# Performance work log

Measured on AMD Instinct MI355X. Metric: run time of the kernel, lower is better.

Reference implementation:

```python
import jax, jax.numpy as jnp
import numpy as np

V, D, H, L, FF, NC = 32000, 512, 8, 4, 2048, 10
HD = D // H
EPS = 1e-5


def _layernorm(x, g, b):
    m = jnp.mean(x, axis=-1, keepdims=True)
    v = jnp.mean((x - m) ** 2, axis=-1, keepdims=True)
    return (x - m) * jax.lax.rsqrt(v + EPS) * g + b


def _pos_encoding(T, d):
    pos = jnp.arange(T, dtype=jnp.float32)[:, None]
    div = jnp.exp(jnp.arange(0, d, 2, dtype=jnp.float32) * (-np.log(10000.0) / d))
    pe = jnp.zeros((T, d), dtype=jnp.float32)
    pe = pe.at[:, 0::2].set(jnp.sin(pos * div))
    pe = pe.at[:, 1::2].set(jnp.cos(pos * div))
    return pe


def setup_inputs() -> dict:
    key = jax.random.key(0)
    ks = iter(jax.random.split(key, 32))
    n = lambda shape, s=0.02: jax.random.normal(next(ks), shape, dtype=jnp.float32) * s
    inp = {
        "tokens": jax.random.randint(next(ks), (8, 1024), 0, V),
        "emb": n((V, D), 1.0),
        # attention projections, stored (in, out) so y = x @ W + b
        "Wq": n((L, D, D)), "bq": jnp.zeros((L, D)),
        "Wk": n((L, D, D)), "bk": jnp.zeros((L, D)),
        "Wv": n((L, D, D)), "bv": jnp.zeros((L, D)),
        "Wo": n((L, D, D)), "bo": jnp.zeros((L, D)),
        "ln1_g": jnp.ones((L, D)), "ln1_b": jnp.zeros((L, D)),
        "ln2_g": jnp.ones((L, D)), "ln2_b": jnp.zeros((L, D)),
        "W1": n((L, D, FF)), "b1": jnp.zeros((L, FF)),
        "W2": n((L, FF, D)), "b2": jnp.zeros((L, D)),
        "heavy_w": n((D, D)), "heavy_b": jnp.zeros((D,)),
        "heavy_a1": n((D, D)), "heavy_a2": n((D, D)),
        "norm_g": jnp.ones((D,)), "norm_b": jnp.zeros((D,)),
        "cls_W": n((D, NC)), "cls_b": jnp.zeros((NC,)),
    }
    return inp


def reference(tokens, emb, Wq, bq, Wk, bk, Wv, bv, Wo, bo,
              ln1_g, ln1_b, ln2_g, ln2_b, W1, b1, W2, b2,
              heavy_w, heavy_b, heavy_a1, heavy_a2,
              norm_g, norm_b, cls_W, cls_b):
    B, T = tokens.shape
    x = emb[tokens] + _pos_encoding(T, D)[None]  # [B,T,D]
    scale = 1.0 / np.sqrt(HD)
    for l in range(L):
        # attention block (pre-norm)
        h = _layernorm(x, ln1_g[l], ln1_b[l])
        q = (h @ Wq[l] + bq[l]).reshape(B, T, H, HD)
        k = (h @ Wk[l] + bk[l]).reshape(B, T, H, HD)
        v = (h @ Wv[l] + bv[l]).reshape(B, T, H, HD)
        scores = jnp.einsum("bqhd,bkhd->bhqk", q, k) * scale
        attn = jax.nn.softmax(scores, axis=-1)
        o = jnp.einsum("bhqk,bkhd->bqhd", attn, v).reshape(B, T, D)
        x = x + (o @ Wo[l] + bo[l])
        # feedforward block
        h = _layernorm(x, ln2_g[l], ln2_b[l])
        x = x + (jax.nn.gelu(h @ W1[l] + b1[l], approximate=False) @ W2[l] + b2[l])
    # heavy layer: chained matmuls + bias + tanh (vectorized over B*T)
    x = jnp.tanh(((x @ heavy_w) @ heavy_a1) @ heavy_a2 + heavy_b)
    x = _layernorm(x, norm_g, norm_b)
    x = jnp.mean(x, axis=1)  # [B,D]
    return x @ cls_W + cls_b  # [B,NC]
```

## Files before the change

kernel.cpp:

```cpp
#include <hip/hip_runtime.h>
#include <math.h>

#define BS   8
#define TT   1024
#define DD   512
#define HH   8
#define LL   4
#define FFD  2048
#define NCC  10
#define MM   (BS*TT)
#define MDl  ((long)MM*DD)

typedef unsigned short u16;
typedef short  short8 __attribute__((ext_vector_type(8)));
typedef float  f32x4  __attribute__((ext_vector_type(4)));
typedef u16    u16x8  __attribute__((ext_vector_type(8)));
typedef u16    u16x4  __attribute__((ext_vector_type(4)));

static __device__ __forceinline__ u16 f2b(float f) {
    union { float f; unsigned u; } x; x.f = f;
    unsigned r = x.u + 0x7FFFu + ((x.u >> 16) & 1u);
    return (u16)(r >> 16);
}
static __device__ __forceinline__ u16 f2b_fast(float f) {
    union { float f; unsigned u; } x; x.f = f;
    return (u16)((x.u + 0x8000u) >> 16);
}
static __device__ __forceinline__ float b2f(u16 u) {
    union { unsigned u; float f; } x; x.u = ((unsigned)u) << 16;
    return x.f;
}

__global__ __launch_bounds__(256)
void embed_kernel(const int* __restrict__ tok, const float* __restrict__ emb,
                  float* __restrict__ X) {
    int i = blockIdx.x * 256 + threadIdx.x;
    int d = i & (DD - 1);
    int row = i >> 9;
    int t = row & (TT - 1);
    int j = d >> 1;
    float freq = __expf((float)(2 * j) * (-9.210340371976184f / 512.0f));
    float ang = (float)t * freq;
    float pe = (d & 1) ? cosf(ang) : sinf(ang);
    X[i] = emb[(long)tok[row] * DD + d] + pe;
}

template<int OUTBF>
__global__ __launch_bounds__(256)
void ln_kernel(const float* __restrict__ in, void* __restrict__ outp,
               const float* __restrict__ g, const float* __restrict__ b) {
    int row = blockIdx.x;
    int tid = threadIdx.x;
    const float* x = in + (long)row * DD;
    float x1 = x[tid], x2 = x[tid + 256];
    __shared__ float red[256], red2[256];
    red[tid] = x1 + x2;
    red2[tid] = x1 * x1 + x2 * x2;
    __syncthreads();
    for (int st = 128; st > 0; st >>= 1) {
        if (tid < st) { red[tid] += red[tid + st]; red2[tid] += red2[tid + st]; }
        __syncthreads();
    }
    float mean = red[0] * (1.0f / DD);
    float var = red2[0] * (1.0f / DD) - mean * mean;
    float rstd = rsqrtf(var + 1e-5f);
    float y1 = (x1 - mean) * rstd * g[tid] + b[tid];
    float y2 = (x2 - mean) * rstd * g[tid + 256] + b[tid + 256];
    if (OUTBF) {
        u16* o = (u16*)outp + (long)row * DD;
        o[tid] = f2b(y1); o[tid + 256] = f2b(y2);
    } else {
        float* o = (float*)outp + (long)row * DD;
        o[tid] = y1; o[tid + 256] = y2;
    }
}

template<int OUTBF, int HAS_BIAS, int ACT, int HAS_RES>
__global__ __launch_bounds__(512, 2)
void mfma_gemm(const u16* __restrict__ A, const u16* __restrict__ BT,
               const float* __restrict__ bias, const float* __restrict__ R,
               void* __restrict__ Cout, int N, int K) {
    __shared__ __align__(16) u16 lds[17408];
    u16* As = lds;
    u16* Bs = lds + 8192;
    const int tid = threadIdx.x;
    const int lane = tid & 63;
    const int w = tid >> 6;
    const int wm = w >> 1;
    const int wn = w & 1;
    const long bm = (long)blockIdx.y * 128;
    const long bn = (long)blockIdx.x * 128;

    f32x4 acc[2][4];
#pragma unroll
    for (int i = 0; i < 2; ++i)
#pragma unroll
        for (int j = 0; j < 4; ++j) acc[i][j] = {0.f, 0.f, 0.f, 0.f};

    const int srow = tid >> 2;
    const int sc0 = (tid & 3) * 2;
    const u16* Ag = A + (bm + srow) * K + sc0 * 8;
    const u16* Bg = BT + (bn + srow) * K + sc0 * 8;
    int soff[2];
#pragma unroll
    for (int j = 0; j < 2; ++j)
        soff[j] = srow * 64 + ((sc0 + j) ^ (srow & 7)) * 8;

    const int fr = lane & 15;
    const int g = lane >> 4;
    const int am0 = wm * 32 + fr;
    const int bn0 = wn * 64 + fr;
    const int sw = fr & 7;

    u16x8 sa[2][2], sb[2][2];
#pragma unroll
    for (int j = 0; j < 2; ++j) {
        sa[0][j] = *(const u16x8*)(Ag + j * 8);
        sb[0][j] = *(const u16x8*)(Bg + j * 8);
    }

    for (int k0 = 0; k0 < K; k0 += 128) {
#pragma unroll
        for (int half = 0; half < 2; ++half) {
            const int cb = half, nb = half ^ 1;
            __syncthreads();
#pragma unroll
            for (int j = 0; j < 2; ++j) {
                *(u16x8*)&As[soff[j]] = sa[cb][j];
                *(u16x8*)&Bs[soff[j]] = sb[cb][j];
            }
            const int knext = k0 + (half + 1) * 64;
            if (knext < K) {
#pragma unroll
                for (int j = 0; j < 2; ++j) {
                    sa[nb][j] = *(const u16x8*)(Ag + knext + j * 8);
                    sb[nb][j] = *(const u16x8*)(Bg + knext + j * 8);
                }
            }
            __syncthreads();
#pragma unroll
            for (int kk = 0; kk < 2; ++kk) {
                const int pos = ((kk << 2) + g) ^ sw;
                short8 af[2], bfv[4];
#pragma unroll
                for (int mi = 0; mi < 2; ++mi)
                    af[mi] = *(const short8*)&As[(am0 + mi * 16) * 64 + pos * 8];
#pragma unroll
                for (int ni = 0; ni < 4; ++ni)
                    bfv[ni] = *(const short8*)&Bs[(bn0 + ni * 16) * 64 + pos * 8];
#pragma unroll
                for (int mi = 0; mi < 2; ++mi)
#pragma unroll
                    for (int ni = 0; ni < 4; ++ni)
                        acc[mi][ni] = __builtin_amdgcn_mfma_f32_16x16x32_bf16(
                            af[mi], bfv[ni], acc[mi][ni], 0, 0, 0);
            }
        }
    }

    const int erow0 = wm * 32 + g * 4;
    const int ecol0 = wn * 64 + fr;

    if (OUTBF) {
        __syncthreads();
#pragma unroll
        for (int ni = 0; ni < 4; ++ni) {
            const long col = bn + ecol0 + ni * 16;
            float bv = 0.f;
            if (HAS_BIAS) bv = bias[col];
#pragma unroll
            for (int mi = 0; mi < 2; ++mi)
#pragma unroll
                for (int r = 0; r < 4; ++r) {
                    const int row = erow0 + mi * 16 + r;
                    float v = acc[mi][ni][r];
                    if (HAS_BIAS) v += bv;
                    if (ACT == 1) v = 0.5f * v * (1.0f + erff(v * 0.70710678118654752f));
                    if (ACT == 2) v = tanhf(v);
                    if (HAS_RES) v += R[(bm + row) * N + col];
                    lds[row * 136 + ecol0 + ni * 16] = f2b(v);
                }
        }
        __syncthreads();
        const int srow2 = tid >> 4;
        const int sch2 = tid & 15;
        u16* Cp = (u16*)Cout;
#pragma unroll
        for (int rr = 0; rr < 4; ++rr) {
            const int row = srow2 + rr * 32;
            u16x8 vv = *(const u16x8*)&lds[row * 136 + sch2 * 8];
            *(u16x8*)(Cp + (bm + row) * N + bn + sch2 * 8) = vv;
        }
    } else {
#pragma unroll
        for (int ni = 0; ni < 4; ++ni) {
            const long col = bn + ecol0 + ni * 16;
            float bv = 0.f;
            if (HAS_BIAS) bv = bias[col];
#pragma unroll
            for (int mi = 0; mi < 2; ++mi)
#pragma unroll
                for (int r = 0; r < 4; ++r) {
                    const long row = bm + erow0 + mi * 16 + r;
                    float v = acc[mi][ni][r];
                    if (HAS_BIAS) v += bv;
                    if (ACT == 1) v = 0.5f * v * (1.0f + erff(v * 0.70710678118654752f));
                    if (ACT == 2) v = tanhf(v);
                    if (HAS_RES) v += R[row * N + col];
                    ((float*)Cout)[row * N + col] = v;
                }
        }
    }
}

__global__ __launch_bounds__(256, 2)
void attn_kernel(const u16* __restrict__ QKV, u16* __restrict__ O) {
    const int id = blockIdx.x;
    const int bh = ((id >> 7) << 3) | (id & 7);
    const int qblk = (id >> 3) & 15;
    const int h = bh & 7;
    const int b = bh >> 3;
    const int tid = threadIdx.x;
    const int lane = tid & 63;
    const int w = tid >> 6;
    const int fr = lane & 15;
    const int g = lane >> 4;

    __shared__ __align__(16) unsigned char smem[20480];
    u16* Vt = (u16*)smem;
    float (*Ored)[16][68] = (float(*)[16][68])smem;
    __shared__ float Lred[4][4][16];

    const long rowb = (long)b * TT;
    const int q0 = qblk * 64;

    short8 qf[4][2];
#pragma unroll
    for (int qt = 0; qt < 4; ++qt)
#pragma unroll
        for (int hf = 0; hf < 2; ++hf)
            qf[qt][hf] = *(const short8*)(QKV + (rowb + q0 + qt * 16 + fr) * 1536
                                          + h * 64 + hf * 32 + g * 8);

    f32x4 accO[4][4];
    float lsum[4];
#pragma unroll
    for (int qt = 0; qt < 4; ++qt) {
        lsum[qt] = 0.f;
#pragma unroll
        for (int nt = 0; nt < 4; ++nt) accO[qt][nt] = {0.f, 0.f, 0.f, 0.f};
    }

    const int vkp = lane & 7;
    const int vd0 = (lane >> 3) * 8;
    u16* Vw0 = Vt + w * 2560;

    auto load_k = [&](int kt_, u16x8* kr_) {
        const u16* kp = QKV + (rowb + (long)kt_ * 64 + w * 16 + fr) * 1536
                        + 512 + h * 64 + g * 8;
        kr_[0] = *(const u16x8*)kp;
        kr_[1] = *(const u16x8*)(kp + 32);
    };
    auto load_v = [&](int kt_, u16x8* vr_) {
        const u16* vp = QKV + (rowb + (long)kt_ * 64 + w * 16 + vkp * 2) * 1536
                        + 1024 + h * 64 + vd0;
        vr_[0] = *(const u16x8*)vp;
        vr_[1] = *(const u16x8*)(vp + 1536);
    };
    auto stage_v = [&](int buf, u16x8* vr_) {
        unsigned* Vt32 = (unsigned*)(Vw0 + buf * 1280);
#pragma unroll
        for (int j = 0; j < 8; ++j)
            Vt32[(vd0 + j) * 10 + vkp] =
                (unsigned)vr_[0][j] | ((unsigned)vr_[1][j] << 16);
    };
    auto compute = [&](int buf, u16x8* kr_) {
        const u16* Vw = Vw0 + buf * 1280;
        short8 vb[4];
#pragma unroll
        for (int nt = 0; nt < 4; ++nt) {
            union { short8 s; u16x4 h2[2]; } u;
            u.h2[0] = *(const u16x4*)(Vw + (nt * 16 + fr) * 20 + g * 4);
            u.h2[1] = (u16x4){0, 0, 0, 0};
            vb[nt] = u.s;
        }
#pragma unroll
        for (int qt = 0; qt < 4; ++qt) {
            f32x4 st = {0.f, 0.f, 0.f, 0.f};
            st = __builtin_amdgcn_mfma_f32_16x16x32_bf16(kr_[0], qf[qt][0], st, 0, 0, 0);
            st = __builtin_amdgcn_mfma_f32_16x16x32_bf16(kr_[1], qf[qt][1], st, 0, 0, 0);
            u16 p0 = f2b_fast(exp2f(st[0] * 0.18033688011112042f));
            u16 p1 = f2b_fast(exp2f(st[1] * 0.18033688011112042f));
            u16 p2 = f2b_fast(exp2f(st[2] * 0.18033688011112042f));
            u16 p3 = f2b_fast(exp2f(st[3] * 0.18033688011112042f));
            lsum[qt] += (b2f(p0) + b2f(p1)) + (b2f(p2) + b2f(p3));
            union { short8 s; unsigned u[4]; } pu;
            pu.u[0] = (unsigned)p0 | ((unsigned)p1 << 16);
            pu.u[1] = (unsigned)p2 | ((unsigned)p3 << 16);
            pu.u[2] = 0; pu.u[3] = 0;
#pragma unroll
            for (int nt = 0; nt < 4; ++nt)
                accO[qt][nt] = __builtin_amdgcn_mfma_f32_16x16x32_bf16(
                    pu.s, vb[nt], accO[qt][nt], 0, 0, 0);
        }
    };

    u16x8 krA[2], vrA[2], krB[2], vrB[2];
    load_k(0, krA); load_v(0, vrA);
    load_k(1, krB); load_v(1, vrB);
    stage_v(0, vrA);

#pragma unroll 1
    for (int kt = 0; kt < 16; kt += 2) {
        stage_v(1, vrB);
        compute(0, krA);
        if (kt + 2 < 16) { load_k(kt + 2, krA); load_v(kt + 2, vrA); }
        compute(1, krB);
        if (kt + 2 < 16) {
            stage_v(0, vrA);
            load_k(kt + 3, krB); load_v(kt + 3, vrB);
        }
    }

#pragma unroll
    for (int qt = 0; qt < 4; ++qt) {
        float s = lsum[qt];
        s += __shfl_xor(s, 16, 64);
        s += __shfl_xor(s, 32, 64);
        Lred[w][qt][fr] = s;
    }
    __syncthreads();

    const int q_ = tid >> 4;
    const int d0 = (tid & 15) * 4;
#pragma unroll
    for (int qt = 0; qt < 4; ++qt) {
#pragma unroll
        for (int nt = 0; nt < 4; ++nt)
#pragma unroll
            for (int r = 0; r < 4; ++r)
                Ored[w][g * 4 + r][nt * 16 + fr] = accO[qt][nt][r];
        __syncthreads();
        f32x4 s = {0.f, 0.f, 0.f, 0.f};
#pragma unroll
        for (int ww = 0; ww < 4; ++ww) {
            f32x4 t = *(const f32x4*)&Ored[ww][q_][d0];
            s[0] += t[0]; s[1] += t[1]; s[2] += t[2]; s[3] += t[3];
        }
        float ltot = Lred[0][qt][q_] + Lred[1][qt][q_]
                   + Lred[2][qt][q_] + Lred[3][qt][q_];
        float rls = 1.0f / ltot;
        long row = rowb + q0 + qt * 16 + q_;
        u16x4 ov;
#pragma unroll
        for (int j = 0; j < 4; ++j) ov[j] = f2b(s[j] * rls);
        *(u16x4*)(O + row * DD + h * 64 + d0) = ov;
        __syncthreads();
    }
}

struct WP   { const float* s; u16* d; };
struct WTbl { WP e[19]; };

__global__ __launch_bounds__(256)
void wprep512_kernel(WTbl tbl) {
    const float* src = tbl.e[blockIdx.z].s;
    u16* dst = tbl.e[blockIdx.z].d;
    int k0 = blockIdx.y * 32, n0 = blockIdx.x * 32;
    __shared__ float tile[32][33];
    int tx = threadIdx.x & 31, ty = threadIdx.x >> 5;
#pragma unroll
    for (int i = 0; i < 4; ++i)
        tile[ty + 8 * i][tx] = src[(long)(k0 + ty + 8 * i) * 512 + n0 + tx];
    __syncthreads();
#pragma unroll
    for (int i = 0; i < 4; ++i) {
        int r = ty + 8 * i;
        dst[(long)(n0 + r) * 512 + k0 + tx] = f2b(tile[tx][r]);
    }
}

__global__ __launch_bounds__(256)
void wprep_kernel(const float* __restrict__ src, u16* __restrict__ dst,
                  int K, int N, long srcLS, long dstLS) {
    int l = blockIdx.z;
    src += (long)l * srcLS;
    dst += (long)l * dstLS;
    int k0 = blockIdx.y * 32, n0 = blockIdx.x * 32;
    __shared__ float tile[32][33];
    int tx = threadIdx.x & 31, ty = threadIdx.x >> 5;
#pragma unroll
    for (int i = 0; i < 4; ++i)
        tile[ty + 8 * i][tx] = src[(long)(k0 + ty + 8 * i) * N + n0 + tx];
    __syncthreads();
#pragma unroll
    for (int i = 0; i < 4; ++i) {
        int r = ty + 8 * i;
        dst[(long)(n0 + r) * K + k0 + tx] = f2b(tile[tx][r]);
    }
}

__global__ __launch_bounds__(256)
void bprep_kernel(const float* __restrict__ bq, const float* __restrict__ bk,
                  const float* __restrict__ bv, float* __restrict__ dst) {
    int i = blockIdx.x * 256 + threadIdx.x;
    int l = i / 1536, j = i - l * 1536;
    float v = (j < 512) ? bq[l * 512 + j]
            : (j < 1024) ? bk[l * 512 + j - 512]
                         : bv[l * 512 + j - 1024];
    dst[i] = v;
}

__global__ __launch_bounds__(256)
void f2b_kernel(const float* __restrict__ in, u16* __restrict__ out, int n) {
    int i = blockIdx.x * 256 + threadIdx.x;
    if (i < n) out[i] = f2b(in[i]);
}

__global__ __launch_bounds__(256)
void zero_kernel(float* __restrict__ p, int n) {
    int i = blockIdx.x * 256 + threadIdx.x;
    if (i < n) p[i] = 0.0f;
}

__global__ __launch_bounds__(256)
void colmean_kernel(const float* __restrict__ Hn, float* __restrict__ XM) {
    int blk = blockIdx.x;
    int b = blk >> 5;
    int r0 = (blk & 31) * 32;
    int tid = threadIdx.x;
    float acc0 = 0.0f, acc1 = 0.0f;
    for (int r = 0; r < 32; ++r) {
        long off = ((long)b * TT + r0 + r) * DD + tid;
        acc0 += Hn[off];
        acc1 += Hn[off + 256];
    }
    atomicAdd(&XM[b * DD + tid], acc0);
    atomicAdd(&XM[b * DD + tid + 256], acc1);
}

__global__ __launch_bounds__(256)
void cls_kernel(const float* __restrict__ XM, const float* __restrict__ W,
                const float* __restrict__ bias, float* __restrict__ out) {
    int b = blockIdx.x;
    int tid = threadIdx.x;
    __shared__ float xm[DD];
    xm[tid] = XM[b * DD + tid] * (1.0f / TT);
    xm[tid + 256] = XM[b * DD + tid + 256] * (1.0f / TT);
    __syncthreads();
    if (tid < NCC) {
        float s = bias[tid];
        for (int d = 0; d < DD; ++d) s += xm[d] * W[d * NCC + tid];
        out[b * NCC + tid] = s;
    }
}

extern "C" void kernel_launch(void* const* d_in, const int* in_sizes, int n_in,
                              void* d_out, int out_size, void* d_ws, size_t ws_size,
                              hipStream_t stream) {
    const int*   tokens  = (const int*)d_in[0];
    const float* emb     = (const float*)d_in[1];
    const float* Wq      = (const float*)d_in[2];
    const float* bq      = (const float*)d_in[3];
    const float* Wk      = (const float*)d_in[4];
    const float* bk      = (const float*)d_in[5];
    const float* Wv      = (const float*)d_in[6];
    const float* bv      = (const float*)d_in[7];
    const float* Wo      = (const float*)d_in[8];
    const float* bo      = (const float*)d_in[9];
    const float* ln1_g   = (const float*)d_in[10];
    const float* ln1_b   = (const float*)d_in[11];
    const float* ln2_g   = (const float*)d_in[12];
    const float* ln2_b   = (const float*)d_in[13];
    const float* W1      = (const float*)d_in[14];
    const float* b1      = (const float*)d_in[15];
    const float* W2      = (const float*)d_in[16];
    const float* b2      = (const float*)d_in[17];
    const float* heavy_w = (const float*)d_in[18];
    const float* heavy_b = (const float*)d_in[19];
    const float* heavy_a1= (const float*)d_in[20];
    const float* heavy_a2= (const float*)d_in[21];
    const float* norm_g  = (const float*)d_in[22];
    const float* norm_b  = (const float*)d_in[23];
    const float* cls_W   = (const float*)d_in[24];
    const float* cls_b   = (const float*)d_in[25];
    float* out = (float*)d_out;

    char* p = (char*)d_ws;
    float* X    = (float*)p;  p += MDl * 4;
    u16*   Hh   = (u16*)p;    p += MDl * 2;
    u16*   QKVb = (u16*)p;
    u16*   FFb  = QKVb;
    u16*   T1   = QKVb;
    u16*   T2   = QKVb + MDl;
    float* LNout= (float*)QKVb;
    p += (long)MM * 1536 * 2;
    u16*   Ob   = (u16*)p;    p += MDl * 2;
    u16*   Xbf  = (u16*)p;    p += MDl * 2;
    u16*   WqkvT= (u16*)p;    p += 4L * 1536 * 512 * 2;
    u16*   WoT  = (u16*)p;    p += 4L * 512 * 512 * 2;
    u16*   W1T  = (u16*)p;    p += 4L * 2048 * 512 * 2;
    u16*   W2T  = (u16*)p;    p += 4L * 512 * 2048 * 2;
    u16*   WhT  = (u16*)p;    p += 3L * 512 * 512 * 2;
    float* bqkv = (float*)p;  p += 4L * 1536 * 4;
    float* XM   = (float*)p;  p += (long)BS * DD * 4;

    dim3 blk(256);
    dim3 blk512(512);

    WTbl tbl;
    for (int l = 0; l < 4; ++l) {
        tbl.e[l * 4 + 0] = {Wq + (long)l * 262144, WqkvT + (long)l * 786432};
        tbl.e[l * 4 + 1] = {Wk + (long)l * 262144, WqkvT + (long)l * 786432 + 262144};
        tbl.e[l * 4 + 2] = {Wv + (long)l * 262144, WqkvT + (long)l * 786432 + 524288};
        tbl.e[l * 4 + 3] = {Wo + (long)l * 262144, WoT + (long)l * 262144};
    }
    tbl.e[16] = {heavy_w,  WhT};
    tbl.e[17] = {heavy_a1, WhT + 262144};
    tbl.e[18] = {heavy_a2, WhT + 524288};
    wprep512_kernel<<<dim3(16, 16, 19), blk, 0, stream>>>(tbl);
    wprep_kernel<<<dim3(64, 16, 4), blk, 0, stream>>>(W1, W1T,  512, 2048, 1048576, 1048576);
    wprep_kernel<<<dim3(16, 64, 4), blk, 0, stream>>>(W2, W2T, 2048,  512, 1048576, 1048576);
    bprep_kernel<<<24, blk, 0, stream>>>(bq, bk, bv, bqkv);

    embed_kernel<<<MM * DD / 256, blk, 0, stream>>>(tokens, emb, X);

    dim3 gQKV(12, 64), g512(4, 64), gFF1(16, 64);

    for (int l = 0; l < LL; ++l) {
        ln_kernel<1><<<MM, blk, 0, stream>>>(X, Hh, ln1_g + l * DD, ln1_b + l * DD);
        mfma_gemm<1, 1, 0, 0><<<gQKV, blk512, 0, stream>>>(
            Hh, WqkvT + (long)l * 786432, bqkv + l * 1536, nullptr, QKVb, 1536, 512);
        attn_kernel<<<dim3(1024), blk, 0, stream>>>(QKVb, Ob);
        mfma_gemm<0, 1, 0, 1><<<g512, blk512, 0, stream>>>(
            Ob, WoT + (long)l * 262144, bo + l * DD, X, X, 512, 512);
        ln_kernel<1><<<MM, blk, 0, stream>>>(X, Hh, ln2_g + l * DD, ln2_b + l * DD);
        mfma_gemm<1, 1, 1, 0><<<gFF1, blk512, 0, stream>>>(
            Hh, W1T + (long)l * 1048576, b1 + l * FFD, nullptr, FFb, 2048, 512);
        mfma_gemm<0, 1, 0, 1><<<g512, blk512, 0, stream>>>(
            FFb, W2T + (long)l * 1048576, b2 + l * DD, X, X, 512, 2048);
    }

    f2b_kernel<<<MM * DD / 256, blk, 0, stream>>>(X, Xbf, MM * DD);
    mfma_gemm<1, 0, 0, 0><<<g512, blk512, 0, stream>>>(Xbf, WhT,          nullptr, nullptr, T1, 512, 512);
    mfma_gemm<1, 0, 0, 0><<<g512, blk512, 0, stream>>>(T1,  WhT + 262144, nullptr, nullptr, T2, 512, 512);
    mfma_gemm<0, 1, 2, 0><<<g512, blk512, 0, stream>>>(T2,  WhT + 524288, heavy_b, nullptr, X,  512, 512);

    ln_kernel<0><<<MM, blk, 0, stream>>>(X, LNout, norm_g, norm_b);
    zero_kernel<<<(BS * DD + 255) / 256, blk, 0, stream>>>(XM, BS * DD);
    colmean_kernel<<<256, blk, 0, stream>>>(LNout, XM);
    cls_kernel<<<BS, blk, 0, stream>>>(XM, cls_W, cls_b, out);
}
```

Measured before the change: 868.3 us.

## Fill full K=32 MFMA in attention PV by pairing key tiles

The attention kernel now processes two 64-key tiles per compute step, so each PV MFMA uses all 32 reduction slots instead of zero-padding half of them. The V shared-memory staging layout is reorganized so each lane reads a full short8 operand, and loads are restructured with a single V register buffer. This halves the PV MFMA count and makes the row sum accumulate from fp32 exponents rather than rounded bf16. In exchange it uses more registers per lane and a larger shared-memory buffer, which may reduce occupancy, and the stage/load ordering with one V buffer is more serialized.

```diff
diff --git a/kernel.cpp b/kernel.cpp
--- a/kernel.cpp
+++ b/kernel.cpp
@@ -226,9 +226,8 @@
     const int fr = lane & 15;
     const int g = lane >> 4;
 
-    __shared__ __align__(16) unsigned char smem[20480];
-    u16* Vt = (u16*)smem;
-    float (*Ored)[16][68] = (float(*)[16][68])smem;
+    __shared__ __align__(16) unsigned Vt32[8192];
+    float (*Ored)[16][68] = (float(*)[16][68])Vt32;
     __shared__ float Lred[4][4][16];
 
     const long rowb = (long)b * TT;
@@ -251,75 +250,84 @@
         for (int nt = 0; nt < 4; ++nt) accO[qt][nt] = {0.f, 0.f, 0.f, 0.f};
     }
 
-    const int vkp = lane & 7;
-    const int vd0 = (lane >> 3) * 8;
-    u16* Vw0 = Vt + w * 2560;
+    const int G = lane & 1;
+    const int kpair = (lane >> 1) & 7;
+    const int dseg = lane >> 4;
+    const int vcol = (kpair >> 1) * 4 + 2 * G + (kpair & 1);
+    unsigned* Vw = Vt32 + w * 2048;
 
     auto load_k = [&](int kt_, u16x8* kr_) {
-        const u16* kp = QKV + (rowb + (long)kt_ * 64 + w * 16 + fr) * 1536
-                        + 512 + h * 64 + g * 8;
-        kr_[0] = *(const u16x8*)kp;
-        kr_[1] = *(const u16x8*)(kp + 32);
+        const u16* kp0 = QKV + (rowb + (long)kt_ * 64 + w * 16 + fr) * 1536
+                         + 512 + h * 64 + g * 8;
+        kr_[0] = *(const u16x8*)kp0;
+        kr_[1] = *(const u16x8*)(kp0 + 32);
+        const u16* kp1 = kp0 + (long)64 * 1536;
+        kr_[2] = *(const u16x8*)kp1;
+        kr_[3] = *(const u16x8*)(kp1 + 32);
     };
     auto load_v = [&](int kt_, u16x8* vr_) {
-        const u16* vp = QKV + (rowb + (long)kt_ * 64 + w * 16 + vkp * 2) * 1536
-                        + 1024 + h * 64 + vd0;
+        const long krow = rowb + (long)(kt_ + G) * 64 + w * 16 + kpair * 2;
+        const u16* vp = QKV + krow * 1536 + 1024 + h * 64 + dseg * 16;
         vr_[0] = *(const u16x8*)vp;
-        vr_[1] = *(const u16x8*)(vp + 1536);
+        vr_[1] = *(const u16x8*)(vp + 8);
+        vr_[2] = *(const u16x8*)(vp + 1536);
+        vr_[3] = *(const u16x8*)(vp + 1536 + 8);
     };
     auto stage_v = [&](int buf, u16x8* vr_) {
-        unsigned* Vt32 = (unsigned*)(Vw0 + buf * 1280);
-#pragma unroll
-        for (int j = 0; j < 8; ++j)
-            Vt32[(vd0 + j) * 10 + vkp] =
-                (unsigned)vr_[0][j] | ((unsigned)vr_[1][j] << 16);
+        unsigned* p = Vw + buf * 1024 + dseg * 16 * 16 + vcol;
+#pragma unroll
+        for (int jj = 0; jj < 8; ++jj)
+            p[jj * 16] = (unsigned)vr_[0][jj] | ((unsigned)vr_[2][jj] << 16);
+#pragma unroll
+        for (int jj = 0; jj < 8; ++jj)
+            p[(8 + jj) * 16] = (unsigned)vr_[1][jj] | ((unsigned)vr_[3][jj] << 16);
     };
-    auto compute = [&](int buf, u16x8* kr_) {
-        const u16* Vw = Vw0 + buf * 1280;
-        short8 vb[4];
-#pragma unroll
-        for (int nt = 0; nt < 4; ++nt) {
-            union { short8 s; u16x4 h2[2]; } u;
-            u.h2[0] = *(const u16x4*)(Vw + (nt * 16 + fr) * 20 + g * 4);
-            u.h2[1] = (u16x4){0, 0, 0, 0};
-            vb[nt] = u.s;
-        }
+    auto compute32 = [&](int buf, u16x8* kr_) {
+        const unsigned* Vb = Vw + buf * 1024;
+        short8 vb0 = *(const short8*)(Vb + (0 * 16 + fr) * 16 + g * 4);
+        short8 vb1 = *(const short8*)(Vb + (1 * 16 + fr) * 16 + g * 4);
+        short8 vb2 = *(const short8*)(Vb + (2 * 16 + fr) * 16 + g * 4);
+        short8 vb3 = *(const short8*)(Vb + (3 * 16 + fr) * 16 + g * 4);
 #pragma unroll
         for (int qt = 0; qt < 4; ++qt) {
-            f32x4 st = {0.f, 0.f, 0.f, 0.f};
-            st = __builtin_amdgcn_mfma_f32_16x16x32_bf16(kr_[0], qf[qt][0], st, 0, 0, 0);
-            st = __builtin_amdgcn_mfma_f32_16x16x32_bf16(kr_[1], qf[qt][1], st, 0, 0, 0);
-            u16 p0 = f2b_fast(exp2f(st[0] * 0.18033688011112042f));
-            u16 p1 = f2b_fast(exp2f(st[1] * 0.18033688011112042f));
-            u16 p2 = f2b_fast(exp2f(st[2] * 0.18033688011112042f));
-            u16 p3 = f2b_fast(exp2f(st[3] * 0.18033688011112042f));
-            lsum[qt] += (b2f(p0) + b2f(p1)) + (b2f(p2) + b2f(p3));
+            f32x4 sa = {0.f, 0.f, 0.f, 0.f}, sb2 = {0.f, 0.f, 0.f, 0.f};
+            sa  = __builtin_amdgcn_mfma_f32_16x16x32_bf16(kr_[0], qf[qt][0], sa, 0, 0, 0);
+            sa  = __builtin_amdgcn_mfma_f32_16x16x32_bf16(kr_[1], qf[qt][1], sa, 0, 0, 0);
+            sb2 = __builtin_amdgcn_mfma_f32_16x16x32_bf16(kr_[2], qf[qt][0], sb2, 0, 0, 0);
+            sb2 = __builtin_amdgcn_mfma_f32_16x16x32_bf16(kr_[3], qf[qt][1], sb2, 0, 0, 0);
+            const float SC = 0.18033688011112042f;
+            float pa0 = exp2f(sa[0] * SC),  pa1 = exp2f(sa[1] * SC);
+            float pa2 = exp2f(sa[2] * SC),  pa3 = exp2f(sa[3] * SC);
+            float pb0 = exp2f(sb2[0] * SC), pb1 = exp2f(sb2[1] * SC);
+            float pb2 = exp2f(sb2[2] * SC), pb3 = exp2f(sb2[3] * SC);
+            lsum[qt] += ((pa0 + pa1) + (pa2 + pa3)) + ((pb0 + pb1) + (pb2 + pb3));
             union { short8 s; unsigned u[4]; } pu;
-            pu.u[0] = (unsigned)p0 | ((unsigned)p1 << 16);
-            pu.u[1] = (unsigned)p2 | ((unsigned)p3 << 16);
-            pu.u[2] = 0; pu.u[3] = 0;
-#pragma unroll
-            for (int nt = 0; nt < 4; ++nt)
-                accO[qt][nt] = __builtin_amdgcn_mfma_f32_16x16x32_bf16(
-                    pu.s, vb[nt], accO[qt][nt], 0, 0, 0);
+            pu.u[0] = (unsigned)f2b_fast(pa0) | ((unsigned)f2b_fast(pa1) << 16);
+            pu.u[1] = (unsigned)f2b_fast(pa2) | ((unsigned)f2b_fast(pa3) << 16);
+            pu.u[2] = (unsigned)f2b_fast(pb0) | ((unsigned)f2b_fast(pb1) << 16);
+            pu.u[3] = (unsigned)f2b_fast(pb2) | ((unsigned)f2b_fast(pb3) << 16);
+            accO[qt][0] = __builtin_amdgcn_mfma_f32_16x16x32_bf16(pu.s, vb0, accO[qt][0], 0, 0, 0);
+            accO[qt][1] = __builtin_amdgcn_mfma_f32_16x16x32_bf16(pu.s, vb1, accO[qt][1], 0, 0, 0);
+            accO[qt][2] = __builtin_amdgcn_mfma_f32_16x16x32_bf16(pu.s, vb2, accO[qt][2], 0, 0, 0);
+            accO[qt][3] = __builtin_amdgcn_mfma_f32_16x16x32_bf16(pu.s, vb3, accO[qt][3], 0, 0, 0);
         }
     };
 
-    u16x8 krA[2], vrA[2], krB[2], vrB[2];
-    load_k(0, krA); load_v(0, vrA);
-    load_k(1, krB); load_v(1, vrB);
-    stage_v(0, vrA);
+    u16x8 krA[4], krB[4], vr[4];
+    load_k(0, krA);  load_v(0, vr);
+    stage_v(0, vr);
+    load_k(2, krB);  load_v(2, vr);
 
 #pragma unroll 1
-    for (int kt = 0; kt < 16; kt += 2) {
-        stage_v(1, vrB);
-        compute(0, krA);
-        if (kt + 2 < 16) { load_k(kt + 2, krA); load_v(kt + 2, vrA); }
-        compute(1, krB);
-        if (kt + 2 < 16) {
-            stage_v(0, vrA);
-            load_k(kt + 3, krB); load_v(kt + 3, vrB);
-        }
+    for (int kt = 0; kt < 16; kt += 4) {
+        stage_v(1, vr);
+        compute32(0, krA);
+        if (kt + 4 < 16) {
+            load_k(kt + 4, krA); load_v(kt + 4, vr);
+            stage_v(0, vr);
+            load_k(kt + 6, krB); load_v(kt + 6, vr);
+        }
+        compute32(1, krB);
     }
 
 #pragma unroll
```

New measurement: 860.6 us. No clear change (-0.9%).
